# Optimization experiments

Measured on AMD Instinct MI355X. Metric: run time of the kernel, lower is better.

Reference implementation:

```python
import jax, jax.numpy as jnp
import numpy as np

B, S, D, H, PF = 2, 2048, 1024, 16, 4096
HD = D // H
EPS = 1e-5


def _rope_tables(seq_len, dim, theta=10000.0):
    freqs = 1.0 / (theta ** (np.arange(0, dim, 2)[: dim // 2].astype(np.float32) / dim))
    ang = np.outer(np.arange(seq_len, dtype=np.float32), freqs)  # [S, D/2]
    return jnp.asarray(np.cos(ang)), jnp.asarray(np.sin(ang))


def setup_inputs() -> dict:
    key = jax.random.key(0)
    ks = jax.random.split(key, 16)
    s = 0.02
    inp = {
        "src": jax.random.normal(ks[0], (B, S, D), dtype=jnp.float32),
        "Wq": jax.random.normal(ks[1], (D, D), dtype=jnp.float32) * s,
        "bq": jnp.zeros((D,), jnp.float32),
        "Wk": jax.random.normal(ks[2], (D, D), dtype=jnp.float32) * s,
        "bk": jnp.zeros((D,), jnp.float32),
        "Wv": jax.random.normal(ks[3], (D, D), dtype=jnp.float32) * s,
        "bv": jnp.zeros((D,), jnp.float32),
        "Wo": jax.random.normal(ks[4], (D, D), dtype=jnp.float32) * s,
        "bo": jnp.zeros((D,), jnp.float32),
        "ln1_g": jnp.ones((D,), jnp.float32),
        "ln1_b": jnp.zeros((D,), jnp.float32),
        "W1": jax.random.normal(ks[5], (D, PF), dtype=jnp.float32) * s,
        "b1": jnp.zeros((PF,), jnp.float32),
        "W2": jax.random.normal(ks[6], (PF, D), dtype=jnp.float32) * s,
        "b2": jnp.zeros((D,), jnp.float32),
        "ln2_g": jnp.ones((D,), jnp.float32),
        "ln2_b": jnp.zeros((D,), jnp.float32),
    }
    cos, sin = _rope_tables(S, D)
    inp["rope_cos"] = cos
    inp["rope_sin"] = sin
    return inp


def _apply_rope(x, cos, sin):
    # x: [B, S, D]; rotate adjacent channel pairs as complex numbers (Meta LLaMA style)
    xp = x.reshape(x.shape[0], x.shape[1], -1, 2)
    a, b = xp[..., 0], xp[..., 1]
    c = cos[None, : x.shape[1]]
    s = sin[None, : x.shape[1]]
    out = jnp.stack([a * c - b * s, a * s + b * c], axis=-1)
    return out.reshape(x.shape)


def _layer_norm(x, g, b):
    mu = x.mean(-1, keepdims=True)
    var = ((x - mu) ** 2).mean(-1, keepdims=True)
    return (x - mu) * jax.lax.rsqrt(var + EPS) * g + b


def reference(src, Wq, bq, Wk, bk, Wv, bv, Wo, bo, ln1_g, ln1_b,
              W1, b1, W2, b2, ln2_g, ln2_b, rope_cos, rope_sin):
    bsz, seq, _ = src.shape
    Q = src @ Wq + bq
    K = src @ Wk + bk
    V = src @ Wv + bv
    Q = _apply_rope(Q, rope_cos, rope_sin)
    K = _apply_rope(K, rope_cos, rope_sin)
    # split heads: [B, H, S, HD]
    Q = Q.reshape(bsz, seq, H, HD).transpose(0, 2, 1, 3)
    K = K.reshape(bsz, seq, H, HD).transpose(0, 2, 1, 3)
    V = V.reshape(bsz, seq, H, HD).transpose(0, 2, 1, 3)
    scale = 1.0 / jnp.sqrt(jnp.float32(HD))
    energy = jnp.einsum("bhqd,bhkd->bhqk", Q, K) * scale
    attn = jax.nn.softmax(energy, axis=-1)
    x = jnp.einsum("bhqk,bhkd->bhqd", attn, V)
    x = x.transpose(0, 2, 1, 3).reshape(bsz, seq, D)
    attn_out = x @ Wo + bo
    # residual + LayerNorm
    h = _layer_norm(src + attn_out, ln1_g, ln1_b)
    # positionwise feedforward
    ff = jax.nn.relu(h @ W1 + b1) @ W2 + b2
    return _layer_norm(h + ff, ln2_g, ln2_b)
```

## Files before the change

### kernel.cpp

```cpp
#include <hip/hip_runtime.h>

#define SEQ 2048
#define DIM 1024
#define NH 16
#define HDIM 64
#define PFF 4096
#define NROWS 4096
#define BATCH 2
#define NQKV 3072

typedef unsigned short u16;
typedef unsigned int u32;
typedef __attribute__((ext_vector_type(8))) short short8;
typedef __attribute__((ext_vector_type(4))) float f32x4;
typedef __attribute__((ext_vector_type(16))) float f32x16;

__device__ inline float b2f(u16 u){ return __uint_as_float(((u32)u)<<16); }
__device__ inline u16 f2b(float f){
  u32 u = __float_as_uint(f);
  u32 r = u + 0x7FFFu + ((u>>16)&1u);
  return (u16)(r>>16);
}

#define AS1C(p) ((const __attribute__((address_space(1))) unsigned int*)(p))
#define AS3P(p) ((__attribute__((address_space(3))) unsigned int*)(p))

__global__ void k_cast_bf16(const float* __restrict__ in, u16* __restrict__ out, int n4){
  int i = blockIdx.x*256 + threadIdx.x;
  if (i >= n4) return;
  float4 v = ((const float4*)in)[i];
  ushort4 o;
  o.x = f2b(v.x); o.y = f2b(v.y); o.z = f2b(v.z); o.w = f2b(v.w);
  ((ushort4*)out)[i] = o;
}

__global__ __launch_bounds__(256) void k_transpose_cast(const float* __restrict__ in,
                                                        u16* __restrict__ out, int R, int C){
  __shared__ float tile[32][33];
  int tx = threadIdx.x & 31, ty = threadIdx.x >> 5;
  int c0 = blockIdx.x*32, r0 = blockIdx.y*32;
  #pragma unroll
  for (int i=0;i<4;++i)
    tile[ty+i*8][tx] = in[(size_t)(r0+ty+i*8)*C + c0 + tx];
  __syncthreads();
  #pragma unroll
  for (int i=0;i<4;++i)
    out[(size_t)(c0+ty+i*8)*R + r0 + tx] = f2b(tile[tx][ty+i*8]);
}

__global__ __launch_bounds__(256) void k_transpose_v(const u16* __restrict__ QKV, u16* __restrict__ VT){
  __shared__ u16 tile[32][34];
  int tx = threadIdx.x & 31, ty = threadIdx.x >> 5;
  int d0 = blockIdx.x*32, r0 = blockIdx.y*32;
  #pragma unroll
  for (int i=0;i<4;++i)
    tile[ty+i*8][tx] = QKV[(size_t)(r0+ty+i*8)*NQKV + 2048 + d0 + tx];
  __syncthreads();
  #pragma unroll
  for (int i=0;i<4;++i)
    VT[(size_t)(d0+ty+i*8)*NROWS + r0 + tx] = tile[tx][ty+i*8];
}

__global__ void k_pack3(const float* __restrict__ a, const float* __restrict__ b,
                        const float* __restrict__ c, float* __restrict__ o){
  int i = blockIdx.x*256 + threadIdx.x;
  if (i >= NQKV) return;
  o[i] = i < 1024 ? a[i] : (i < 2048 ? b[i-1024] : c[i-2048]);
}

template<bool RELU, bool BF16OUT>
__global__ __launch_bounds__(512, 2) void k_gemm256(
    const u16* __restrict__ A, const u16* __restrict__ Bt,
    const float* __restrict__ bias, void* __restrict__ Cp,
    int M, int N, int K, int lda, int ldb){
  extern __shared__ char lds[];
  const int tid = threadIdx.x;
  const int lane = tid & 63, wid = tid >> 6;
  const int quad = lane >> 4, l15 = lane & 15;
  const int wm = wid >> 2, wn = wid & 3;
  const int ro = (l15*4 + quad)*16;
  const int srow = lane >> 2;
  const int sk   = (lane & 3)*8;
  const int nwg = gridDim.x * gridDim.y;
  int lid = blockIdx.y * gridDim.x + blockIdx.x;
  lid = (lid & 7) * (nwg >> 3) + (lid >> 3);
  const int bx = lid % gridDim.x, by = lid / gridDim.x;
  const int rowBase = by*256, colBase = bx*256;

  f32x4 acc[8][4] = {};

  auto stage2 = [&](int buf, int k0, int i){
    int idx = i*8 + wid;
    int rs = idx >> 1, ks = idx & 1;
    const u16* ga = A + (size_t)(rowBase + rs*16 + srow)*lda + k0 + ks*32 + sk;
    __builtin_amdgcn_global_load_lds(AS1C(ga), AS3P(lds + buf*65536 + idx*1024), 16, 0, 0);
    const u16* gb = Bt + (size_t)(colBase + rs*16 + srow)*ldb + k0 + ks*32 + sk;
    __builtin_amdgcn_global_load_lds(AS1C(gb), AS3P(lds + buf*65536 + 32768 + idx*1024), 16, 0, 0);
  };

  #pragma unroll
  for (int i=0;i<4;++i) stage2(0, 0, i);
  __syncthreads();

  const int NT = K >> 6;
  #pragma unroll 1
  for (int t=0; t<NT; ++t){
    const int buf = t & 1;
    const bool pf = (t+1 < NT);
    const int k0n = (t+1)*64;
    char* Ab = lds + buf*65536;
    char* Bb = Ab + 32768;
    short8 a0[4][2], a1[4][2], b0[2][2], b1[2][2];

    #pragma unroll
    for (int mf=0; mf<4; ++mf)
      #pragma unroll
      for (int kk=0; kk<2; ++kk)
        a0[mf][kk] = *(const short8*)(Ab + ((wm*8+mf)*2+kk)*1024 + ro);
    #pragma unroll
    for (int nf=0; nf<2; ++nf)
      #pragma unroll
      for (int kk=0; kk<2; ++kk)
        b0[nf][kk] = *(const short8*)(Bb + ((wn*4+nf)*2+kk)*1024 + ro);
    if (pf){ stage2(buf^1, k0n, 0); stage2(buf^1, k0n, 1); }
    __builtin_amdgcn_s_barrier();
    __builtin_amdgcn_s_setprio(1);
    #pragma unroll
    for (int mf=0; mf<4; ++mf)
      #pragma unroll
      for (int nf=0; nf<2; ++nf)
        #pragma unroll
        for (int kk=0; kk<2; ++kk)
          acc[mf][nf] = __builtin_amdgcn_mfma_f32_16x16x32_bf16(a0[mf][kk], b0[nf][kk], acc[mf][nf], 0,0,0);
    __builtin_amdgcn_s_setprio(0);
    __builtin_amdgcn_s_barrier();

    #pragma unroll
    for (int nf=0; nf<2; ++nf)
      #pragma unroll
      for (int kk=0; kk<2; ++kk)
        b1[nf][kk] = *(const short8*)(Bb + ((wn*4+2+nf)*2+kk)*1024 + ro);
    if (pf){ stage2(buf^1, k0n, 2); stage2(buf^1, k0n, 3); }
    __builtin_amdgcn_s_barrier();
    __builtin_amdgcn_s_setprio(1);
    #pragma unroll
    for (int mf=0; mf<4; ++mf)
      #pragma unroll
      for (int nf=0; nf<2; ++nf)
        #pragma unroll
        for (int kk=0; kk<2; ++kk)
          acc[mf][2+nf] = __builtin_amdgcn_mfma_f32_16x16x32_bf16(a0[mf][kk], b1[nf][kk], acc[mf][2+nf], 0,0,0);
    __builtin_amdgcn_s_setprio(0);
    __builtin_amdgcn_s_barrier();

    #pragma unroll
    for (int mf=0; mf<4; ++mf)
      #pragma unroll
      for (int kk=0; kk<2; ++kk)
        a1[mf][kk] = *(const short8*)(Ab + ((wm*8+4+mf)*2+kk)*1024 + ro);
    __builtin_amdgcn_s_barrier();
    __builtin_amdgcn_s_setprio(1);
    #pragma unroll
    for (int mf=0; mf<4; ++mf)
      #pragma unroll
      for (int nf=0; nf<2; ++nf)
        #pragma unroll
        for (int kk=0; kk<2; ++kk)
          acc[4+mf][2+nf] = __builtin_amdgcn_mfma_f32_16x16x32_bf16(a1[mf][kk], b1[nf][kk], acc[4+mf][2+nf], 0,0,0);
    __builtin_amdgcn_s_setprio(0);
    __builtin_amdgcn_s_barrier();

    if (pf) asm volatile("s_waitcnt vmcnt(0)" ::: "memory");
    __builtin_amdgcn_s_barrier();
    __builtin_amdgcn_s_setprio(1);
    #pragma unroll
    for (int mf=0; mf<4; ++mf)
      #pragma unroll
      for (int nf=0; nf<2; ++nf)
        #pragma unroll
        for (int kk=0; kk<2; ++kk)
          acc[4+mf][nf] = __builtin_amdgcn_mfma_f32_16x16x32_bf16(a1[mf][kk], b0[nf][kk], acc[4+mf][nf], 0,0,0);
    __builtin_amdgcn_s_setprio(0);
    __builtin_amdgcn_s_barrier();
  }

  #pragma unroll
  for (int mf=0; mf<8; ++mf){
    #pragma unroll
    for (int nf=0; nf<4; ++nf){
      int col = colBase + wn*64 + nf*16 + l15;
      float bv = bias[col];
      #pragma unroll
      for (int j=0; j<4; ++j){
        int row = rowBase + wm*128 + mf*16 + quad*4 + j;
        float v = acc[mf][nf][j] + bv;
        if (RELU) v = fmaxf(v, 0.f);
        if (BF16OUT) ((u16*)Cp)[(size_t)row*N + col] = f2b(v);
        else         ((float*)Cp)[(size_t)row*N + col] = v;
      }
    }
  }
}

template<bool RELU, bool BF16OUT, bool BIAS>
__global__ __launch_bounds__(256) void k_gemm(
    const u16* __restrict__ A, const u16* __restrict__ Bt,
    const float* __restrict__ bias, void* __restrict__ Cp,
    int M, int N, int Kc, int lda, int ldb){
  __shared__ __align__(16) char lds[32768];
  const int tid = threadIdx.x;
  const int lane = tid & 63, wid = tid >> 6;
  const int quad = lane >> 4, l15 = lane & 15;
  const int wr = wid >> 1, wc = wid & 1;
  const int nwg = gridDim.x * gridDim.y;
  int lid = blockIdx.y * gridDim.x + blockIdx.x;
  lid = (lid & 7) * (nwg >> 3) + (lid >> 3);
  const int bx = lid % gridDim.x, by = lid / gridDim.x;
  const int rowBase = by * 128, colBase = bx * 128;
  const u16* Az = A  + (size_t)blockIdx.z * Kc;
  const u16* Bz = Bt + (size_t)blockIdx.z * Kc;
  f32x4 acc[4][4] = {};
  const int srow = lane >> 3;
  const int scol = lane & 7;
  for (int k0 = 0; k0 < Kc; k0 += 64) {
    __syncthreads();
    #pragma unroll
    for (int i=0;i<4;++i){
      int wch = wid*4 + i;
      int row = wch*8 + srow;
      int c   = scol ^ (row & 7);
      const u16* ga = Az + (size_t)(rowBase+row)*lda + k0 + c*8;
      __builtin_amdgcn_global_load_lds(AS1C(ga), AS3P(lds + wch*1024), 16, 0, 0);
      const u16* gb = Bz + (size_t)(colBase+row)*ldb + k0 + c*8;
      __builtin_amdgcn_global_load_lds(AS1C(gb), AS3P(lds + 16384 + wch*1024), 16, 0, 0);
    }
    __syncthreads();
    #pragma unroll
    for (int kk=0;kk<2;++kk){
      short8 af[4], bfr[4];
      #pragma unroll
      for (int m=0;m<4;++m){
        int r = wr*64 + m*16 + l15;
        af[m] = *(const short8*)(lds + ((r*128 + kk*64 + quad*16) ^ ((r&7)<<4)));
      }
      #pragma unroll
      for (int n=0;n<4;++n){
        int r = wc*64 + n*16 + l15;
        bfr[n] = *(const short8*)(lds + 16384 + ((r*128 + kk*64 + quad*16) ^ ((r&7)<<4)));
      }
      __builtin_amdgcn_s_setprio(1);
      #pragma unroll
      for (int m=0;m<4;++m)
        #pragma unroll
        for (int n=0;n<4;++n)
          acc[m][n] = __builtin_amdgcn_mfma_f32_16x16x32_bf16(af[m], bfr[n], acc[m][n], 0,0,0);
      __builtin_amdgcn_s_setprio(0);
    }
  }
  float* Cf = (float*)Cp + (size_t)blockIdx.z * M * N;
  #pragma unroll
  for (int m=0;m<4;++m){
    #pragma unroll
    for (int n=0;n<4;++n){
      int col = colBase + wc*64 + n*16 + l15;
      float bv = (BIAS && blockIdx.z == 0) ? bias[col] : 0.f;
      #pragma unroll
      for (int j=0;j<4;++j){
        int row = rowBase + wr*64 + m*16 + quad*4 + j;
        float v = acc[m][n][j] + bv;
        if (RELU) v = fmaxf(v, 0.f);
        if (BF16OUT) ((u16*)Cp)[(size_t)row*N + col] = f2b(v);
        else         Cf[(size_t)row*N + col] = v;
      }
    }
  }
}

__global__ void k_rope(u16* __restrict__ QKV,
                       const float* __restrict__ cosT, const float* __restrict__ sinT){
  int idx = blockIdx.x*256 + threadIdx.x;
  int row = idx >> 9, p = idx & 511;
  int s = row & (SEQ-1);
  float c = cosT[s*512 + p], sn = sinT[s*512 + p];
  u16* qp = QKV + (size_t)row*NQKV + 2*p;
  u16* kp = qp + 1024;
  ushort2 q = *(ushort2*)qp;
  ushort2 k = *(ushort2*)kp;
  float qx = b2f(q.x), qy = b2f(q.y), kx = b2f(k.x), ky = b2f(k.y);
  const float scale = 0.125f;
  ushort2 qo, ko;
  qo.x = f2b((qx*c - qy*sn)*scale);
  qo.y = f2b((qx*sn + qy*c)*scale);
  ko.x = f2b(kx*c - ky*sn);
  ko.y = f2b(kx*sn + ky*c);
  *(ushort2*)qp = qo;
  *(ushort2*)kp = ko;
}

__global__ __launch_bounds__(256) void k_attn(
    const u16* __restrict__ QKV, const u16* __restrict__ VT, u16* __restrict__ Xo){
  const int qt = blockIdx.x, h = blockIdx.y, b = blockIdx.z;
  const int tid = threadIdx.x, lane = tid & 63, wid = tid >> 6;
  const int l31 = lane & 31, hi = lane >> 5;
  __shared__ __align__(16) char lds[32768];
  const int srow = lane >> 3, scol = lane & 7;

  short8 qf[4];
  {
    const u16* qrow = QKV + (size_t)(b*SEQ + qt*128 + wid*32 + l31)*NQKV + h*HDIM;
    #pragma unroll
    for (int dk=0; dk<4; ++dk)
      qf[dk] = *(const short8*)(qrow + dk*16 + 8*hi);
  }
  float m_run = -1e30f, s_run = 0.f;
  f32x16 oacc[2] = {};
  const size_t krow0 = (size_t)(b*SEQ);

  auto do_stage = [&](int buf, int kt){
    char* kdst = lds + buf*16384;
    char* vdst = kdst + 8192;
    #pragma unroll
    for (int i=0;i<2;++i){
      int wch = wid*2 + i;
      int row = wch*8 + srow;
      int c = scol ^ (row & 7);
      const u16* gk = QKV + (krow0 + kt*64 + row)*NQKV + 1024 + h*HDIM + c*8;
      __builtin_amdgcn_global_load_lds(AS1C(gk), AS3P(kdst + wch*1024), 16, 0, 0);
      const u16* gv = VT + (size_t)(h*HDIM + row)*NROWS + b*SEQ + kt*64 + c*8;
      __builtin_amdgcn_global_load_lds(AS1C(gv), AS3P(vdst + wch*1024), 16, 0, 0);
    }
  };

  auto do_tile = [&](int buf){
    char* kb = lds + buf*16384;
    char* vb = kb + 8192;
    f32x16 pacc[2] = {};
    __builtin_amdgcn_s_setprio(1);
    #pragma unroll
    for (int kbk=0;kbk<2;++kbk){
      #pragma unroll
      for (int dk=0;dk<4;++dk){
        int row = kbk*32 + l31;
        short8 kf = *(const short8*)(kb + ((row*128 + dk*32 + 16*hi) ^ ((row&7)<<4)));
        pacc[kbk] = __builtin_amdgcn_mfma_f32_32x32x16_bf16(kf, qf[dk], pacc[kbk], 0,0,0);
      }
    }
    __builtin_amdgcn_s_setprio(0);
    float tmax = -1e30f;
    #pragma unroll
    for (int kbk=0;kbk<2;++kbk)
      #pragma unroll
      for (int r=0;r<16;++r) tmax = fmaxf(tmax, pacc[kbk][r]);
    tmax = fmaxf(tmax, __shfl_xor(tmax, 32));
    if (__any(tmax > m_run + 8.0f)){
      float mnew = fmaxf(m_run, tmax);
      float a = __expf(m_run - mnew);
      s_run *= a;
      m_run = mnew;
      #pragma unroll
      for (int r=0;r<16;++r){
        int src = (r&3) + 8*(r>>2) + 4*hi;
        float ar = __shfl(a, src);
        oacc[0][r] *= ar;
        oacc[1][r] *= ar;
      }
    }
    float p[2][16];
    float psum = 0.f;
    #pragma unroll
    for (int kbk=0;kbk<2;++kbk)
      #pragma unroll
      for (int r=0;r<16;++r){
        float e = __expf(pacc[kbk][r] - m_run);
        p[kbk][r] = e;
        psum += e;
      }
    psum += __shfl_xor(psum, 32);
    s_run += psum;
    short8 pa[4];
    #pragma unroll
    for (int kbk=0;kbk<2;++kbk){
      #pragma unroll
      for (int s=0;s<2;++s){
        u32 X0, X1, Y0, Y1;
        asm("v_cvt_pk_bf16_f32 %0, %1, %2" : "=v"(X0) : "v"(p[kbk][8*s+0]), "v"(p[kbk][8*s+1]));
        asm("v_cvt_pk_bf16_f32 %0, %1, %2" : "=v"(X1) : "v"(p[kbk][8*s+2]), "v"(p[kbk][8*s+3]));
        asm("v_cvt_pk_bf16_f32 %0, %1, %2" : "=v"(Y0) : "v"(p[kbk][8*s+4]), "v"(p[kbk][8*s+5]));
        asm("v_cvt_pk_bf16_f32 %0, %1, %2" : "=v"(Y1) : "v"(p[kbk][8*s+6]), "v"(p[kbk][8*s+7]));
        asm volatile("v_permlane32_swap_b32 %0, %1" : "+v"(X0), "+v"(Y0));
        asm volatile("v_permlane32_swap_b32 %0, %1" : "+v"(X1), "+v"(Y1));
        union { u32 w[4]; short8 s8; } pu;
        pu.w[0] = X0; pu.w[1] = X1; pu.w[2] = Y0; pu.w[3] = Y1;
        pa[2*kbk+s] = pu.s8;
      }
    }
    __builtin_amdgcn_s_setprio(1);
    #pragma unroll
    for (int db=0;db<2;++db){
      #pragma unroll
      for (int ks=0;ks<4;++ks){
        int row = db*32 + l31;
        short8 vf = *(const short8*)(vb + ((row*128 + ks*32 + 16*hi) ^ ((row&7)<<4)));
        oacc[db] = __builtin_amdgcn_mfma_f32_32x32x16_bf16(pa[ks], vf, oacc[db], 0,0,0);
      }
    }
    __builtin_amdgcn_s_setprio(0);
  };

  do_stage(0, 0);
  __syncthreads();
  const int NT = SEQ/64;
  #pragma unroll 1
  for (int kt=0; kt<NT; kt+=2){
    do_stage(1, kt+1);
    do_tile(0);
    __syncthreads();
    if (kt+2 < NT) do_stage(0, kt+2);
    do_tile(1);
    __syncthreads();
  }
  #pragma unroll
  for (int r=0;r<16;++r){
    int crow = (r&3) + 8*(r>>2) + 4*hi;
    float sq = __shfl(s_run, crow);
    float rs = __builtin_amdgcn_rcpf(sq);
    int grow = b*SEQ + qt*128 + wid*32 + crow;
    Xo[(size_t)grow*DIM + h*HDIM + l31]      = f2b(oacc[0][r] * rs);
    Xo[(size_t)grow*DIM + h*HDIM + 32 + l31] = f2b(oacc[1][r] * rs);
  }
}

template<int PARTS, bool WBF>
__global__ __launch_bounds__(256) void k_ln(
    const float* __restrict__ a, const float* __restrict__ p0, const float* __restrict__ p1,
    const float* __restrict__ g, const float* __restrict__ be,
    float* __restrict__ outf, u16* __restrict__ outb){
  const int row = blockIdx.x, tid = threadIdx.x;
  __shared__ float red[8];
  float4 av = ((const float4*)(a  + (size_t)row*DIM))[tid];
  float4 b0 = ((const float4*)(p0 + (size_t)row*DIM))[tid];
  float4 b1 = ((const float4*)(p1 + (size_t)row*DIM))[tid];
  float x0 = av.x+b0.x+b1.x, x1 = av.y+b0.y+b1.y, x2 = av.z+b0.z+b1.z, x3 = av.w+b0.w+b1.w;
  float s = x0+x1+x2+x3;
  #pragma unroll
  for (int o=32;o>=1;o>>=1) s += __shfl_down(s, o);
  if ((tid&63)==0) red[tid>>6] = s;
  __syncthreads();
  float mean = (red[0]+red[1]+red[2]+red[3]) * (1.0f/DIM);
  float d0=x0-mean, d1=x1-mean, d2=x2-mean, d3=x3-mean;
  float vs = d0*d0+d1*d1+d2*d2+d3*d3;
  #pragma unroll
  for (int o=32;o>=1;o>>=1) vs += __shfl_down(vs, o);
  if ((tid&63)==0) red[4+(tid>>6)] = vs;
  __syncthreads();
  float var = (red[4]+red[5]+red[6]+red[7]) * (1.0f/DIM);
  float rs = rsqrtf(var + 1e-5f);
  float4 gv = ((const float4*)g)[tid];
  float4 bev = ((const float4*)be)[tid];
  float4 y;
  y.x = d0*rs*gv.x + bev.x;
  y.y = d1*rs*gv.y + bev.y;
  y.z = d2*rs*gv.z + bev.z;
  y.w = d3*rs*gv.w + bev.w;
  ((float4*)(outf + (size_t)row*DIM))[tid] = y;
  if (WBF){
    ushort4 o4; o4.x=f2b(y.x); o4.y=f2b(y.y); o4.z=f2b(y.z); o4.w=f2b(y.w);
    ((ushort4*)(outb + (size_t)row*DIM))[tid] = o4;
  }
}

extern "C" void kernel_launch(void* const* d_in, const int* in_sizes, int n_in,
                              void* d_out, int out_size, void* d_ws, size_t ws_size,
                              hipStream_t stream){
  (void)in_sizes; (void)n_in; (void)out_size; (void)ws_size;
  const float* src  = (const float*)d_in[0];
  const float* Wq   = (const float*)d_in[1];
  const float* bq   = (const float*)d_in[2];
  const float* Wk   = (const float*)d_in[3];
  const float* bk   = (const float*)d_in[4];
  const float* Wv   = (const float*)d_in[5];
  const float* bv   = (const float*)d_in[6];
  const float* Wo   = (const float*)d_in[7];
  const float* bo   = (const float*)d_in[8];
  const float* ln1g = (const float*)d_in[9];
  const float* ln1b = (const float*)d_in[10];
  const float* W1   = (const float*)d_in[11];
  const float* b1   = (const float*)d_in[12];
  const float* W2   = (const float*)d_in[13];
  const float* b2   = (const float*)d_in[14];
  const float* ln2g = (const float*)d_in[15];
  const float* ln2b = (const float*)d_in[16];
  const float* rc   = (const float*)d_in[17];
  const float* rsn  = (const float*)d_in[18];

  char* ws = (char*)d_ws;
  const size_t MB = (size_t)1<<20;
  u16* Xbf   = (u16*)(ws);
  u16* QKV   = (u16*)(ws + 8*MB);
  u16* VTb   = (u16*)(ws + 32*MB);
  float* aop   = (float*)(ws + 8*MB);
  float* ff2p  = (float*)(ws + 8*MB);
  u16* xat   = (u16*)(ws + 40*MB);
  u16* hbf   = (u16*)(ws + 48*MB);
  u16* WqkvT = (u16*)(ws + 56*MB);
  u16* WoT   = (u16*)(ws + 62*MB);
  u16* W1T   = (u16*)(ws + 64*MB);
  u16* W2T   = (u16*)(ws + 72*MB);
  u16* ff1   = (u16*)(ws + 80*MB);
  float* h   = (float*)(ws + 112*MB);
  float* bqkv= (float*)(ws + 128*MB);
  const size_t P16 = 16*MB/4;

  hipFuncSetAttribute((const void*)&k_gemm256<false,true>,
                      hipFuncAttributeMaxDynamicSharedMemorySize, 131072);
  hipFuncSetAttribute((const void*)&k_gemm256<true,true>,
                      hipFuncAttributeMaxDynamicSharedMemorySize, 131072);

  dim3 blk(256);
  k_cast_bf16<<<dim3(NROWS*DIM/1024), blk, 0, stream>>>(src, Xbf, NROWS*DIM/4);
  k_transpose_cast<<<dim3(DIM/32, DIM/32), blk, 0, stream>>>(Wq, WqkvT, DIM, DIM);
  k_transpose_cast<<<dim3(DIM/32, DIM/32), blk, 0, stream>>>(Wk, WqkvT + (size_t)1024*1024, DIM, DIM);
  k_transpose_cast<<<dim3(DIM/32, DIM/32), blk, 0, stream>>>(Wv, WqkvT + (size_t)2048*1024, DIM, DIM);
  k_transpose_cast<<<dim3(DIM/32, DIM/32), blk, 0, stream>>>(Wo, WoT, DIM, DIM);
  k_transpose_cast<<<dim3(PFF/32, DIM/32), blk, 0, stream>>>(W1, W1T, DIM, PFF);
  k_transpose_cast<<<dim3(DIM/32, PFF/32), blk, 0, stream>>>(W2, W2T, PFF, DIM);
  k_pack3<<<dim3(12), blk, 0, stream>>>(bq, bk, bv, bqkv);

  k_gemm256<false,true><<<dim3(NQKV/256, NROWS/256), dim3(512), 131072, stream>>>(
      Xbf, WqkvT, bqkv, QKV, NROWS, NQKV, DIM, DIM, DIM);
  k_rope<<<dim3(NROWS*512/256), blk, 0, stream>>>(QKV, rc, rsn);
  k_transpose_v<<<dim3(DIM/32, NROWS/32), blk, 0, stream>>>(QKV, VTb);
  k_attn<<<dim3(SEQ/128, NH, BATCH), blk, 0, stream>>>(QKV, VTb, xat);
  k_gemm<false,false,true><<<dim3(DIM/128, NROWS/128, 2), blk, 0, stream>>>(
      xat, WoT, bo, aop, NROWS, DIM, 512, DIM, DIM);
  k_ln<2,true><<<dim3(NROWS), blk, 0, stream>>>(src, aop, aop + P16, ln1g, ln1b, h, hbf);
  k_gemm256<true,true><<<dim3(PFF/256, NROWS/256), dim3(512), 131072, stream>>>(
      hbf, W1T, b1, ff1, NROWS, PFF, DIM, DIM, DIM);
  k_gemm<false,false,true><<<dim3(DIM/128, NROWS/128, 2), blk, 0, stream>>>(
      ff1, W2T, b2, ff2p, NROWS, DIM, 2048, PFF, PFF);
  k_ln<2,false><<<dim3(NROWS), blk, 0, stream>>>(h, ff2p, ff2p + P16, ln2g, ln2b, (float*)d_out, nullptr);
}
```

Before: 255.4 us.

## Use 256-tile split-K GEMM for FFN down-projection, exp2 softmax with max3

Routes the FFN second GEMM through the larger 256x256 tile kernel, now split four ways along K, with bf16 partial outputs. A new LayerNorm kernel sums the four partials and adds the residual. The attention softmax folds log2(e) into the Q scale during RoPE, then uses a raw v_exp_f32 and v_max3 reductions. Storing partials in bf16 loses precision before the sum, and four partials add extra memory traffic.

New measurement: 250.8 us. Within noise of the previous version (-1.8%).

```diff
diff --git a/kernel.cpp b/kernel.cpp
--- a/kernel.cpp
+++ b/kernel.cpp
@@ -21,6 +21,12 @@
   u32 r = u + 0x7FFFu + ((u>>16)&1u);
   return (u16)(r>>16);
 }
+__device__ __forceinline__ float fexp2(float x){
+  float r; asm("v_exp_f32 %0, %1" : "=v"(r) : "v"(x)); return r;
+}
+__device__ __forceinline__ float fmax3(float a, float b, float c){
+  float r; asm("v_max3_f32 %0, %1, %2, %3" : "=v"(r) : "v"(a), "v"(b), "v"(c)); return r;
+}
 
 #define AS1C(p) ((const __attribute__((address_space(1))) unsigned int*)(p))
 #define AS3P(p) ((__attribute__((address_space(3))) unsigned int*)(p))
@@ -68,11 +74,11 @@
   o[i] = i < 1024 ? a[i] : (i < 2048 ? b[i-1024] : c[i-2048]);
 }
 
-template<bool RELU, bool BF16OUT>
+template<bool RELU, bool BF16OUT, int SPLIT>
 __global__ __launch_bounds__(512, 2) void k_gemm256(
     const u16* __restrict__ A, const u16* __restrict__ Bt,
     const float* __restrict__ bias, void* __restrict__ Cp,
-    int M, int N, int K, int lda, int ldb){
+    int M, int N, int Kc, int lda, int ldb){
   extern __shared__ char lds[];
   const int tid = threadIdx.x;
   const int lane = tid & 63, wid = tid >> 6;
@@ -86,15 +92,17 @@
   lid = (lid & 7) * (nwg >> 3) + (lid >> 3);
   const int bx = lid % gridDim.x, by = lid / gridDim.x;
   const int rowBase = by*256, colBase = bx*256;
+  const u16* Az = A  + (size_t)blockIdx.z * Kc;
+  const u16* Bz = Bt + (size_t)blockIdx.z * Kc;
 
   f32x4 acc[8][4] = {};
 
   auto stage2 = [&](int buf, int k0, int i){
     int idx = i*8 + wid;
     int rs = idx >> 1, ks = idx & 1;
-    const u16* ga = A + (size_t)(rowBase + rs*16 + srow)*lda + k0 + ks*32 + sk;
+    const u16* ga = Az + (size_t)(rowBase + rs*16 + srow)*lda + k0 + ks*32 + sk;
     __builtin_amdgcn_global_load_lds(AS1C(ga), AS3P(lds + buf*65536 + idx*1024), 16, 0, 0);
-    const u16* gb = Bt + (size_t)(colBase + rs*16 + srow)*ldb + k0 + ks*32 + sk;
+    const u16* gb = Bz + (size_t)(colBase + rs*16 + srow)*ldb + k0 + ks*32 + sk;
     __builtin_amdgcn_global_load_lds(AS1C(gb), AS3P(lds + buf*65536 + 32768 + idx*1024), 16, 0, 0);
   };
 
@@ -102,7 +110,7 @@
   for (int i=0;i<4;++i) stage2(0, 0, i);
   __syncthreads();
 
-  const int NT = K >> 6;
+  const int NT = Kc >> 6;
   #pragma unroll 1
   for (int t=0; t<NT; ++t){
     const int buf = t & 1;
@@ -184,19 +192,21 @@
     __builtin_amdgcn_s_barrier();
   }
 
+  u16* Cb = (u16*)Cp + (SPLIT > 1 ? (size_t)blockIdx.z * M * N : 0);
+  float* Cf = (float*)Cp + (SPLIT > 1 ? (size_t)blockIdx.z * M * N : 0);
   #pragma unroll
   for (int mf=0; mf<8; ++mf){
     #pragma unroll
     for (int nf=0; nf<4; ++nf){
       int col = colBase + wn*64 + nf*16 + l15;
-      float bv = bias[col];
+      float bv = (SPLIT == 1 || blockIdx.z == 0) ? bias[col] : 0.f;
       #pragma unroll
       for (int j=0; j<4; ++j){
         int row = rowBase + wm*128 + mf*16 + quad*4 + j;
         float v = acc[mf][nf][j] + bv;
         if (RELU) v = fmaxf(v, 0.f);
-        if (BF16OUT) ((u16*)Cp)[(size_t)row*N + col] = f2b(v);
-        else         ((float*)Cp)[(size_t)row*N + col] = v;
+        if (BF16OUT) Cb[(size_t)row*N + col] = f2b(v);
+        else         Cf[(size_t)row*N + col] = v;
       }
     }
   }
@@ -287,7 +297,7 @@
   ushort2 q = *(ushort2*)qp;
   ushort2 k = *(ushort2*)kp;
   float qx = b2f(q.x), qy = b2f(q.y), kx = b2f(k.x), ky = b2f(k.y);
-  const float scale = 0.125f;
+  const float scale = 0.125f * 1.44269504f;
   ushort2 qo, ko;
   qo.x = f2b((qx*c - qy*sn)*scale);
   qo.y = f2b((qx*sn + qy*c)*scale);
@@ -346,15 +356,15 @@
       }
     }
     __builtin_amdgcn_s_setprio(0);
-    float tmax = -1e30f;
-    #pragma unroll
-    for (int kbk=0;kbk<2;++kbk)
-      #pragma unroll
-      for (int r=0;r<16;++r) tmax = fmaxf(tmax, pacc[kbk][r]);
+    float tmax = fmaxf(pacc[0][0], pacc[0][1]);
+    #pragma unroll
+    for (int r=2;r<16;r+=2) tmax = fmax3(tmax, pacc[0][r], pacc[0][r+1]);
+    #pragma unroll
+    for (int r=0;r<16;r+=2) tmax = fmax3(tmax, pacc[1][r], pacc[1][r+1]);
     tmax = fmaxf(tmax, __shfl_xor(tmax, 32));
     if (__any(tmax > m_run + 8.0f)){
       float mnew = fmaxf(m_run, tmax);
-      float a = __expf(m_run - mnew);
+      float a = fexp2(m_run - mnew);
       s_run *= a;
       m_run = mnew;
       #pragma unroll
@@ -371,7 +381,7 @@
     for (int kbk=0;kbk<2;++kbk)
       #pragma unroll
       for (int r=0;r<16;++r){
-        float e = __expf(pacc[kbk][r] - m_run);
+        float e = fexp2(pacc[kbk][r] - m_run);
         p[kbk][r] = e;
         psum += e;
       }
@@ -467,6 +477,44 @@
     ushort4 o4; o4.x=f2b(y.x); o4.y=f2b(y.y); o4.z=f2b(y.z); o4.w=f2b(y.w);
     ((ushort4*)(outb + (size_t)row*DIM))[tid] = o4;
   }
+}
+
+template<int PARTS>
+__global__ __launch_bounds__(256) void k_lnp(
+    const float* __restrict__ a, const u16* __restrict__ p,
+    const float* __restrict__ g, const float* __restrict__ be,
+    float* __restrict__ outf){
+  const int row = blockIdx.x, tid = threadIdx.x;
+  __shared__ float red[8];
+  float4 av = ((const float4*)(a + (size_t)row*DIM))[tid];
+  float x0 = av.x, x1 = av.y, x2 = av.z, x3 = av.w;
+  #pragma unroll
+  for (int z=0; z<PARTS; ++z){
+    ushort4 pv = ((const ushort4*)(p + (size_t)z*NROWS*DIM + (size_t)row*DIM))[tid];
+    x0 += b2f(pv.x); x1 += b2f(pv.y); x2 += b2f(pv.z); x3 += b2f(pv.w);
+  }
+  float s = x0+x1+x2+x3;
+  #pragma unroll
+  for (int o=32;o>=1;o>>=1) s += __shfl_down(s, o);
+  if ((tid&63)==0) red[tid>>6] = s;
+  __syncthreads();
+  float mean = (red[0]+red[1]+red[2]+red[3]) * (1.0f/DIM);
+  float d0=x0-mean, d1=x1-mean, d2=x2-mean, d3=x3-mean;
+  float vs = d0*d0+d1*d1+d2*d2+d3*d3;
+  #pragma unroll
+  for (int o=32;o>=1;o>>=1) vs += __shfl_down(vs, o);
+  if ((tid&63)==0) red[4+(tid>>6)] = vs;
+  __syncthreads();
+  float var = (red[4]+red[5]+red[6]+red[7]) * (1.0f/DIM);
+  float rs = rsqrtf(var + 1e-5f);
+  float4 gv = ((const float4*)g)[tid];
+  float4 bev = ((const float4*)be)[tid];
+  float4 y;
+  y.x = d0*rs*gv.x + bev.x;
+  y.y = d1*rs*gv.y + bev.y;
+  y.z = d2*rs*gv.z + bev.z;
+  y.w = d3*rs*gv.w + bev.w;
+  ((float4*)(outf + (size_t)row*DIM))[tid] = y;
 }
 
 extern "C" void kernel_launch(void* const* d_in, const int* in_sizes, int n_in,
@@ -499,7 +547,7 @@
   u16* QKV   = (u16*)(ws + 8*MB);
   u16* VTb   = (u16*)(ws + 32*MB);
   float* aop   = (float*)(ws + 8*MB);
-  float* ff2p  = (float*)(ws + 8*MB);
+  u16* ff2b  = (u16*)(ws + 8*MB);
   u16* xat   = (u16*)(ws + 40*MB);
   u16* hbf   = (u16*)(ws + 48*MB);
   u16* WqkvT = (u16*)(ws + 56*MB);
@@ -511,9 +559,11 @@
   float* bqkv= (float*)(ws + 128*MB);
   const size_t P16 = 16*MB/4;
 
-  hipFuncSetAttribute((const void*)&k_gemm256<false,true>,
+  hipFuncSetAttribute((const void*)&k_gemm256<false,true,1>,
                       hipFuncAttributeMaxDynamicSharedMemorySize, 131072);
-  hipFuncSetAttribute((const void*)&k_gemm256<true,true>,
+  hipFuncSetAttribute((const void*)&k_gemm256<true,true,1>,
+                      hipFuncAttributeMaxDynamicSharedMemorySize, 131072);
+  hipFuncSetAttribute((const void*)&k_gemm256<false,true,4>,
                       hipFuncAttributeMaxDynamicSharedMemorySize, 131072);
 
   dim3 blk(256);
@@ -526,7 +576,7 @@
   k_transpose_cast<<<dim3(DIM/32, PFF/32), blk, 0, stream>>>(W2, W2T, PFF, DIM);
   k_pack3<<<dim3(12), blk, 0, stream>>>(bq, bk, bv, bqkv);
 
-  k_gemm256<false,true><<<dim3(NQKV/256, NROWS/256), dim3(512), 131072, stream>>>(
+  k_gemm256<false,true,1><<<dim3(NQKV/256, NROWS/256), dim3(512), 131072, stream>>>(
       Xbf, WqkvT, bqkv, QKV, NROWS, NQKV, DIM, DIM, DIM);
   k_rope<<<dim3(NROWS*512/256), blk, 0, stream>>>(QKV, rc, rsn);
   k_transpose_v<<<dim3(DIM/32, NROWS/32), blk, 0, stream>>>(QKV, VTb);
@@ -534,9 +584,9 @@
   k_gemm<false,false,true><<<dim3(DIM/128, NROWS/128, 2), blk, 0, stream>>>(
       xat, WoT, bo, aop, NROWS, DIM, 512, DIM, DIM);
   k_ln<2,true><<<dim3(NROWS), blk, 0, stream>>>(src, aop, aop + P16, ln1g, ln1b, h, hbf);
-  k_gemm256<true,true><<<dim3(PFF/256, NROWS/256), dim3(512), 131072, stream>>>(
+  k_gemm256<true,true,1><<<dim3(PFF/256, NROWS/256), dim3(512), 131072, stream>>>(
       hbf, W1T, b1, ff1, NROWS, PFF, DIM, DIM, DIM);
-  k_gemm<false,false,true><<<dim3(DIM/128, NROWS/128, 2), blk, 0, stream>>>(
-      ff1, W2T, b2, ff2p, NROWS, DIM, 2048, PFF, PFF);
-  k_ln<2,false><<<dim3(NROWS), blk, 0, stream>>>(h, ff2p, ff2p + P16, ln2g, ln2b, (float*)d_out, nullptr);
-}
+  k_gemm256<false,true,4><<<dim3(DIM/256, NROWS/256, 4), dim3(512), 131072, stream>>>(
+      ff1, W2T, b2, ff2b, NROWS, DIM, 1024, PFF, PFF);
+  k_lnp<4><<<dim3(NROWS), blk, 0, stream>>>(h, ff2b, ln2g, ln2b, (float*)d_out);
+}
```
